# Kernel optimization log

Measured on AMD Instinct MI355X. Metric: run time of the kernel, lower is better.

Reference implementation:

```python
import jax, jax.numpy as jnp
import numpy as np

E = 16        # n_experts
N = 4         # n_mhc
D = 512       # d_hidden
D_FFN = int(D * 1.618)  # 828
TOP_PROB = 0.8
MAX_K = 4
SINKHORN_ITERS = 6
EPS = 1e-8


def top_prob_max_k(logits, threshold=TOP_PROB, max_k=MAX_K):
    probs = jax.nn.softmax(logits, axis=-1)
    order = jnp.argsort(-probs, axis=-1)                       # descending sort indices
    sorted_p = jnp.take_along_axis(probs, order, axis=-1)
    cumsum = jnp.cumsum(sorted_p, axis=-1)
    ar = jnp.arange(logits.shape[-1])
    mask = (cumsum - sorted_p < threshold) & (ar < max_k)
    mask = mask.at[..., 0].set(True)
    selected = sorted_p * mask.astype(probs.dtype)
    inv = jnp.argsort(order, axis=-1)                          # inverse permutation == scatter
    return jnp.take_along_axis(selected, inv, axis=-1)


def sinkhorn_knopp(M, n_iters=SINKHORN_ITERS):
    M = jnp.exp(M)
    for _ in range(n_iters):
        M = M / M.sum(axis=-1, keepdims=True)
        M = M / M.sum(axis=-2, keepdims=True)
    return M


def setup_inputs() -> dict:
    key = jax.random.key(0)
    ks = jax.random.split(key, 12)
    nd = N * D
    inp = {
        'stream': jax.random.normal(ks[0], (2, N, 1024, D), dtype=jnp.float32),
        # BatchedMHC params
        'norm_w': jnp.ones((E, nd), dtype=jnp.float32),
        'phi_pre_w': jax.random.normal(ks[1], (E, N, nd), dtype=jnp.float32) * 0.01,
        'phi_post_w': jax.random.normal(ks[2], (E, N, nd), dtype=jnp.float32) * 0.01,
        'phi_res_w': jax.random.normal(ks[3], (E, N * N, nd), dtype=jnp.float32) * 0.01,
        'b_pre': jnp.zeros((E, N), dtype=jnp.float32),
        'b_post': jnp.zeros((E, N), dtype=jnp.float32),
        'b_res': jnp.zeros((E, N, N), dtype=jnp.float32),
        'alpha_pre': jnp.ones((E,), dtype=jnp.float32),
        'alpha_post': jnp.ones((E,), dtype=jnp.float32),
        'alpha_res': jnp.ones((E,), dtype=jnp.float32),
        # SwiGLU expert params
        'swiglu_norm_w': jnp.ones((E, D), dtype=jnp.float32),
        'swiglu_wd_w': jax.random.normal(ks[4], (E, D, D), dtype=jnp.float32) * 0.01,
        'swiglu_wu_w': jax.random.normal(ks[5], (E, D, D), dtype=jnp.float32) * 0.01,
        'swiglu_gate_w': jax.random.normal(ks[6], (E, D_FFN, D), dtype=jnp.float32) * 0.01,
        'swiglu_up_w': jax.random.normal(ks[7], (E, D_FFN, D), dtype=jnp.float32) * 0.01,
        'swiglu_down_w': jax.random.normal(ks[8], (E, D, D_FFN), dtype=jnp.float32) * 0.01,
        # router (nn.Linear without bias): logits = x @ W.T, W: (E, D)
        'router_w': jax.random.normal(ks[9], (E, D), dtype=jnp.float32) * (1.0 / np.sqrt(D)),
    }
    return inp


def reference(stream, norm_w, phi_pre_w, phi_post_w, phi_res_w,
              b_pre, b_post, b_res, alpha_pre, alpha_post, alpha_res,
              swiglu_norm_w, swiglu_wd_w, swiglu_wu_w,
              swiglu_gate_w, swiglu_up_w, swiglu_down_w, router_w):
    B, n, T, d = stream.shape
    nd = n * d

    # ---- routing (eval mode: no gumbel) ----
    route_input = stream.mean(axis=1)                               # (B,T,d)
    router_logits = jnp.einsum('btd,ed->bte', route_input, router_w)
    gate_moe = top_prob_max_k(router_logits)                        # (B,T,E)
    router_probs = jax.nn.softmax(router_logits, axis=-1)
    moe_mask = (gate_moe > 0).astype(router_probs.dtype)
    route_lp = (jnp.maximum(jnp.log(router_probs), -10.0) * moe_mask).sum(-1)  # (B,T)

    # Original gathers active experts (always excluding expert 0) and skips gate==0
    # experts; since gate_e multiplies each expert's output, computing all experts
    # 1..E-1 is mathematically identical. K = E-1.
    sl = slice(1, E)

    # ---- BatchedMHC ----
    x = stream.transpose(0, 2, 1, 3).reshape(B, T, nd)              # (B,T,nd)
    rms = jax.lax.rsqrt(jnp.mean(x * x, axis=-1, keepdims=True) + EPS)
    xn = x * rms                                                    # (B,T,nd)
    # fold per-expert norm weight into the phi projections (avoids K*B*T*nd tensor)
    phi_pre_eff = phi_pre_w[sl] * norm_w[sl, None, :]               # (K,n,nd)
    phi_post_eff = phi_post_w[sl] * norm_w[sl, None, :]
    phi_res_eff = phi_res_w[sl] * norm_w[sl, None, :]               # (K,n*n,nd)

    H_pre = jax.nn.sigmoid(alpha_pre[sl, None, None, None]
                           * jnp.einsum('btd,knd->kbtn', xn, phi_pre_eff)
                           + b_pre[sl, None, None, :])              # (K,B,T,n)
    H_post = 2.0 * jax.nn.sigmoid(alpha_post[sl, None, None, None]
                                  * jnp.einsum('btd,knd->kbtn', xn, phi_post_eff)
                                  + b_post[sl, None, None, :])      # (K,B,T,n)
    res_e = jnp.einsum('btd,knd->kbtn', xn, phi_res_eff)
    K = E - 1
    H_res_raw = (alpha_res[sl].reshape(K, 1, 1, 1, 1)
                 * res_e.reshape(K, B, T, n, n)
                 + b_res[sl, None, None, :, :])
    H_res = sinkhorn_knopp(H_res_raw)                               # (K,B,T,n,n)

    # ---- per-expert SwiGLU ----
    h_e = jnp.einsum('kbtn,bntd->kbtd', H_pre, stream)              # (K,B,T,d)
    rms2 = jax.lax.rsqrt(jnp.mean(h_e * h_e, axis=-1, keepdims=True) + EPS)
    h = h_e * rms2 * swiglu_norm_w[sl, None, None, :]

    wd_out = jnp.einsum('kbtd,kod->kbto', h, swiglu_wd_w[sl])
    g = jax.nn.sigmoid(jnp.einsum('kbtd,kod->kbto', jax.nn.silu(wd_out), swiglu_wu_w[sl]))
    gate_out = jnp.einsum('kbtd,kod->kbto', h, swiglu_gate_w[sl])   # (K,B,T,d_ffn)
    up_out = jnp.einsum('kbtd,kod->kbto', h, swiglu_up_w[sl])
    out_e = g * jnp.einsum('kbtf,kof->kbto', jax.nn.silu(gate_out) * up_out,
                           swiglu_down_w[sl])                        # (K,B,T,d)

    # ---- combine ----
    gate_4d = gate_moe[:, :, 1:].transpose(2, 0, 1)[:, :, None, :, None]  # (K,B,1,T,1)
    res = jnp.einsum('kbtij,bjtd->kbitd', H_res, stream)            # (K,B,n,T,d)
    post = jnp.einsum('kbtn,kbtd->kbntd', H_post, out_e)            # (K,B,n,T,d)
    stream_update = (gate_4d * (res + post)).sum(axis=0)            # (B,n,T,d)

    return stream_update, gate_moe, route_lp
```

## Files before the change

### kernel.cpp

```cpp
#include <hip/hip_runtime.h>
#include <hip/hip_bf16.h>
#include <math.h>

typedef __attribute__((ext_vector_type(8))) short short8;
typedef __attribute__((ext_vector_type(4))) float floatx4;

#define T_LEN 1024
#define D_H 512
#define ND 2048
#define KEXP 15
#define DFFN 828
#define DFFN_P 896
#define BT_TOT 2048
#define PHI_ROWS 360
#define PHI_ROWS_P 384
#define PAIR_CAP 8320

#define WD_OFF   0
#define WU_OFF   262144
#define GATE_OFF 524288
#define UP_OFF   983040
#define DOWN_OFF 1441792
#define EXPW     1900544

__device__ __forceinline__ float sigmoidf_(float x) { return 1.f / (1.f + expf(-x)); }
__device__ __forceinline__ unsigned short bf16b_(float x) {
    __hip_bfloat16 h = __float2bfloat16(x);
    return *reinterpret_cast<unsigned short*>(&h);
}

__global__ __launch_bounds__(64) void router_kernel(
    const float* __restrict__ stream, const float* __restrict__ rw,
    float* __restrict__ gate_out, float* __restrict__ lp_out,
    int* __restrict__ cnt, int* __restrict__ list, int* __restrict__ pos)
{
    int bt = blockIdx.x; int b = bt >> 10; int t = bt & 1023;
    int lane = threadIdx.x;
    float ri[8];
#pragma unroll
    for (int w = 0; w < 8; ++w) {
        int d = lane + w * 64;
        float s = 0.f;
#pragma unroll
        for (int n = 0; n < 4; ++n)
            s += stream[(((size_t)b * 4 + n) * T_LEN + t) * D_H + d];
        ri[w] = 0.25f * s;
    }
    float logits[16];
    for (int e = 0; e < 16; ++e) {
        float p = 0.f;
#pragma unroll
        for (int w = 0; w < 8; ++w) p += ri[w] * rw[e * D_H + lane + w * 64];
#pragma unroll
        for (int off = 32; off; off >>= 1) p += __shfl_xor(p, off, 64);
        logits[e] = p;
    }
    float mx = logits[0];
    for (int e = 1; e < 16; ++e) mx = fmaxf(mx, logits[e]);
    float pr[16]; float sum = 0.f;
    for (int e = 0; e < 16; ++e) { pr[e] = expf(logits[e] - mx); sum += pr[e]; }
    float inv = 1.f / sum;
    for (int e = 0; e < 16; ++e) pr[e] *= inv;

    float gate[16]; bool taken[16];
    for (int e = 0; e < 16; ++e) { gate[e] = 0.f; taken[e] = false; }
    float prefix = 0.f;
    for (int rank = 0; rank < 4; ++rank) {
        int best = -1; float bp = -1.f;
        for (int e = 0; e < 16; ++e)
            if (!taken[e] && pr[e] > bp) { bp = pr[e]; best = e; }
        taken[best] = true;
        bool sel = (rank == 0) || (prefix < 0.8f);
        if (sel) gate[best] = bp;
        prefix += bp;
        if (!sel) break;
    }
    float lp = 0.f;
    for (int e = 0; e < 16; ++e)
        if (gate[e] > 0.f) lp += fmaxf(logf(pr[e]), -10.f);
    if (lane < 16) gate_out[(size_t)bt * 16 + lane] = gate[lane];
    if (lane == 0) lp_out[bt] = lp;
    if (lane >= 1 && lane < 16 && gate[lane] > 0.f) {
        int k = lane - 1;
        int p = atomicAdd(&cnt[k], 1);
        list[k * BT_TOT + p] = bt;
        pos[k * BT_TOT + bt] = p;
    }
}

__global__ void scan_kernel(const int* __restrict__ cnt, int* __restrict__ offs) {
    if (threadIdx.x == 0) {
        int a = 0;
        for (int k = 0; k < KEXP; ++k) { offs[k] = a; a += cnt[k]; }
        offs[KEXP] = a;
    }
}

__global__ __launch_bounds__(256) void xn_kernel(
    const float* __restrict__ stream, __hip_bfloat16* __restrict__ xn)
{
    int bt = blockIdx.x; int b = bt >> 10; int t = bt & 1023;
    int tid = threadIdx.x;
    float v[8]; float ss = 0.f;
#pragma unroll
    for (int w = 0; w < 8; ++w) {
        int j = tid + w * 256;
        int n = j >> 9, d = j & 511;
        float x = stream[(((size_t)b * 4 + n) * T_LEN + t) * D_H + d];
        v[w] = x; ss += x * x;
    }
#pragma unroll
    for (int off = 32; off; off >>= 1) ss += __shfl_down(ss, off, 64);
    __shared__ float red[4];
    int wave = tid >> 6, lane = tid & 63;
    if (lane == 0) red[wave] = ss;
    __syncthreads();
    float tot = red[0] + red[1] + red[2] + red[3];
    float r = rsqrtf(tot / (float)ND + 1e-8f);
#pragma unroll
    for (int w = 0; w < 8; ++w)
        xn[(size_t)bt * ND + tid + w * 256] = __float2bfloat16(v[w] * r);
}

__global__ __launch_bounds__(256) void cvt_phi_kernel(
    const float* __restrict__ norm_w, const float* __restrict__ phi_pre,
    const float* __restrict__ phi_post, const float* __restrict__ phi_res,
    __hip_bfloat16* __restrict__ phi_all)
{
    int idx = blockIdx.x * 256 + threadIdx.x;
    int row = idx >> 11, col = idx & 2047;
    float v = 0.f;
    if (row < PHI_ROWS) {
        int k = row / 24, j = row - k * 24, e = k + 1;
        float nw = norm_w[(size_t)e * ND + col];
        float p;
        if (j < 4)      p = phi_pre[((size_t)e * 4 + j) * ND + col];
        else if (j < 8) p = phi_post[((size_t)e * 4 + (j - 4)) * ND + col];
        else            p = phi_res[((size_t)e * 16 + (j - 8)) * ND + col];
        v = p * nw;
    }
    phi_all[idx] = __float2bfloat16(v);
}

__global__ __launch_bounds__(256) void cvt_all_kernel(
    const float* __restrict__ wd, const float* __restrict__ wu,
    const float* __restrict__ gate, const float* __restrict__ up,
    const float* __restrict__ down, __hip_bfloat16* __restrict__ wbuf, int e0)
{
    int z = blockIdx.z;
    int type = blockIdx.y;
    int g = blockIdx.x * 256 + threadIdx.x;
    int e = e0 + z;
    __hip_bfloat16* dstb = wbuf + (size_t)z * EXPW;
    float4 v = make_float4(0.f, 0.f, 0.f, 0.f);
    size_t didx;
    if (type <= 1) {
        if (g >= 65536) return;
        didx = (type == 0 ? WD_OFF : WU_OFF) + (size_t)g * 4;
        const float* src = (type == 0 ? wd : wu) + (size_t)e * 262144;
        v = *(const float4*)(src + (size_t)g * 4);
    } else if (type <= 3) {
        if (g >= 114688) return;
        size_t idx4 = (size_t)g * 4;
        didx = (type == 2 ? GATE_OFF : UP_OFF) + idx4;
        if (idx4 < (size_t)DFFN * 512) {
            const float* src = (type == 2 ? gate : up) + (size_t)e * DFFN * 512;
            v = *(const float4*)(src + idx4);
        }
    } else {
        if (g >= 114688) return;
        int r = g / 224, gc = g - r * 224;
        didx = DOWN_OFF + (size_t)g * 4;
        if (gc < 207)
            v = *(const float4*)(down + (size_t)e * 512 * DFFN + (size_t)r * DFFN + gc * 4);
    }
    ushort4 o;
    o.x = bf16b_(v.x); o.y = bf16b_(v.y); o.z = bf16b_(v.z); o.w = bf16b_(v.w);
    *(ushort4*)((unsigned short*)dstb + didx) = o;
}

#define BM 128
#define BN 128
#define BK 32
#define LDSS 40
__global__ __launch_bounds__(256) void gemm_mfma(
    const __hip_bfloat16* __restrict__ A, const __hip_bfloat16* __restrict__ W,
    float* __restrict__ Cf, int Ka, int Oc, int kLen, int kzStride)
{
    __shared__ __align__(16) unsigned short As[BM * LDSS];
    __shared__ __align__(16) unsigned short Ws[BN * LDSS];
    int z = blockIdx.z;
    int bo = blockIdx.x * BN;
    int bm = blockIdx.y * BM;
    int kbeg = z * kzStride;
    int tid = threadIdx.x;
    int wid = tid >> 6, lane = tid & 63;
    int quad = lane >> 4, lr = lane & 15;
    int wm = (wid & 1) * 64, wn = (wid >> 1) * 64;
    int srow = tid >> 2;
    int schk = (tid & 3) * 8;

    floatx4 acc[4][4];
#pragma unroll
    for (int i = 0; i < 4; ++i)
#pragma unroll
        for (int j = 0; j < 4; ++j) { floatx4 zv = {0.f, 0.f, 0.f, 0.f}; acc[i][j] = zv; }

    for (int k0 = kbeg; k0 < kbeg + kLen; k0 += BK) {
        float4 a0 = *(const float4*)(A + (size_t)(bm + srow) * Ka + k0 + schk);
        float4 a1 = *(const float4*)(A + (size_t)(bm + srow + 64) * Ka + k0 + schk);
        float4 w0 = *(const float4*)(W + (size_t)(bo + srow) * Ka + k0 + schk);
        float4 w1 = *(const float4*)(W + (size_t)(bo + srow + 64) * Ka + k0 + schk);
        __syncthreads();
        *(float4*)&As[srow * LDSS + schk] = a0;
        *(float4*)&As[(srow + 64) * LDSS + schk] = a1;
        *(float4*)&Ws[srow * LDSS + schk] = w0;
        *(float4*)&Ws[(srow + 64) * LDSS + schk] = w1;
        __syncthreads();
        short8 af[4], bf[4];
#pragma unroll
        for (int mi = 0; mi < 4; ++mi)
            af[mi] = *(const short8*)&As[(wm + mi * 16 + lr) * LDSS + quad * 8];
#pragma unroll
        for (int ni = 0; ni < 4; ++ni)
            bf[ni] = *(const short8*)&Ws[(wn + ni * 16 + lr) * LDSS + quad * 8];
#pragma unroll
        for (int mi = 0; mi < 4; ++mi)
#pragma unroll
            for (int ni = 0; ni < 4; ++ni)
                acc[mi][ni] = __builtin_amdgcn_mfma_f32_16x16x32_bf16(
                    af[mi], bf[ni], acc[mi][ni], 0, 0, 0);
    }
#pragma unroll
    for (int mi = 0; mi < 4; ++mi) {
        int row0 = bm + wm + mi * 16 + quad * 4;
#pragma unroll
        for (int ni = 0; ni < 4; ++ni) {
            int col = bo + wn + ni * 16 + lr;
#pragma unroll
            for (int r = 0; r < 4; ++r)
                atomicAdd(&Cf[(size_t)(row0 + r) * Oc + col], acc[mi][ni][r]);
        }
    }
}

__global__ __launch_bounds__(256) void gemm_fused(
    const __hip_bfloat16* __restrict__ A, const __hip_bfloat16* __restrict__ wbuf,
    __hip_bfloat16* __restrict__ s1A, __hip_bfloat16* __restrict__ tA,
    const int* __restrict__ counts, const int* __restrict__ offs, int kg)
{
    __shared__ __align__(16) unsigned short As[BM * LDSS];
    __shared__ __align__(16) unsigned short Gs[BN * LDSS];
    __shared__ __align__(16) unsigned short Us[BN * LDSS];
    int z = blockIdx.z;
    int k = kg + z;
    int bm = blockIdx.y * BM;
    if (bm >= counts[k]) return;
    int base = offs[k];
    bool dual = (blockIdx.x >= 4);
    int bo = dual ? (blockIdx.x - 4) * BN : blockIdx.x * BN;
    const __hip_bfloat16* Ab = A + (size_t)base * D_H;
    const __hip_bfloat16* W1 = wbuf + (size_t)z * EXPW + (dual ? GATE_OFF : WD_OFF);
    const __hip_bfloat16* W2 = wbuf + (size_t)z * EXPW + UP_OFF;
    int tid = threadIdx.x;
    int wid = tid >> 6, lane = tid & 63;
    int quad = lane >> 4, lr = lane & 15;
    int wm = (wid & 1) * 64, wn = (wid >> 1) * 64;
    int srow = tid >> 2;
    int schk = (tid & 3) * 8;

    floatx4 a1[4][4], a2[4][4];
#pragma unroll
    for (int i = 0; i < 4; ++i)
#pragma unroll
        for (int j = 0; j < 4; ++j) {
            floatx4 zv = {0.f, 0.f, 0.f, 0.f};
            a1[i][j] = zv; a2[i][j] = zv;
        }

    for (int k0 = 0; k0 < D_H; k0 += BK) {
        float4 x0 = *(const float4*)(Ab + (size_t)(bm + srow) * D_H + k0 + schk);
        float4 x1 = *(const float4*)(Ab + (size_t)(bm + srow + 64) * D_H + k0 + schk);
        float4 g0 = *(const float4*)(W1 + (size_t)(bo + srow) * D_H + k0 + schk);
        float4 g1 = *(const float4*)(W1 + (size_t)(bo + srow + 64) * D_H + k0 + schk);
        float4 u0, u1;
        if (dual) {
            u0 = *(const float4*)(W2 + (size_t)(bo + srow) * D_H + k0 + schk);
            u1 = *(const float4*)(W2 + (size_t)(bo + srow + 64) * D_H + k0 + schk);
        }
        __syncthreads();
        *(float4*)&As[srow * LDSS + schk] = x0;
        *(float4*)&As[(srow + 64) * LDSS + schk] = x1;
        *(float4*)&Gs[srow * LDSS + schk] = g0;
        *(float4*)&Gs[(srow + 64) * LDSS + schk] = g1;
        if (dual) {
            *(float4*)&Us[srow * LDSS + schk] = u0;
            *(float4*)&Us[(srow + 64) * LDSS + schk] = u1;
        }
        __syncthreads();
        short8 af[4], bg[4];
#pragma unroll
        for (int mi = 0; mi < 4; ++mi)
            af[mi] = *(const short8*)&As[(wm + mi * 16 + lr) * LDSS + quad * 8];
#pragma unroll
        for (int ni = 0; ni < 4; ++ni)
            bg[ni] = *(const short8*)&Gs[(wn + ni * 16 + lr) * LDSS + quad * 8];
#pragma unroll
        for (int mi = 0; mi < 4; ++mi)
#pragma unroll
            for (int ni = 0; ni < 4; ++ni)
                a1[mi][ni] = __builtin_amdgcn_mfma_f32_16x16x32_bf16(
                    af[mi], bg[ni], a1[mi][ni], 0, 0, 0);
        if (dual) {
            short8 bu[4];
#pragma unroll
            for (int ni = 0; ni < 4; ++ni)
                bu[ni] = *(const short8*)&Us[(wn + ni * 16 + lr) * LDSS + quad * 8];
#pragma unroll
            for (int mi = 0; mi < 4; ++mi)
#pragma unroll
                for (int ni = 0; ni < 4; ++ni)
                    a2[mi][ni] = __builtin_amdgcn_mfma_f32_16x16x32_bf16(
                        af[mi], bu[ni], a2[mi][ni], 0, 0, 0);
        }
    }

#pragma unroll
    for (int mi = 0; mi < 4; ++mi) {
        int row0 = bm + wm + mi * 16 + quad * 4;
#pragma unroll
        for (int ni = 0; ni < 4; ++ni) {
            int col = bo + wn + ni * 16 + lr;
#pragma unroll
            for (int r = 0; r < 4; ++r) {
                float v = a1[mi][ni][r];
                if (dual) {
                    float uu = a2[mi][ni][r];
                    tA[(size_t)(base + row0 + r) * DFFN_P + col] =
                        __float2bfloat16(v * sigmoidf_(v) * uu);
                } else {
                    s1A[(size_t)(base + row0 + r) * D_H + col] =
                        __float2bfloat16(v * sigmoidf_(v));
                }
            }
        }
    }
}

#define BM64 64
__global__ __launch_bounds__(256) void gemm_mfma64(
    const __hip_bfloat16* __restrict__ A, const __hip_bfloat16* __restrict__ W,
    const __hip_bfloat16* __restrict__ aux, __hip_bfloat16* __restrict__ C,
    const int* __restrict__ counts, const int* __restrict__ offs, int kg,
    int Ka, int Oc, size_t woff, int epi)
{
    __shared__ __align__(16) unsigned short As[BM64 * LDSS];
    __shared__ __align__(16) unsigned short Ws[BN * LDSS];
    int z = blockIdx.z;
    int k = kg + z;
    int bm = blockIdx.y * BM64;
    if (bm >= counts[k]) return;
    int base = offs[k];
    int bo = blockIdx.x * BN;
    const __hip_bfloat16* Ab = A + (size_t)base * Ka;
    const __hip_bfloat16* Wg = W + (size_t)z * EXPW + woff;
    int tid = threadIdx.x;
    int wid = tid >> 6, lane = tid & 63;
    int quad = lane >> 4, lr = lane & 15;
    int wm = (wid & 1) * 32, wn = (wid >> 1) * 64;
    int srow = tid >> 2;
    int schk = (tid & 3) * 8;

    floatx4 acc[2][4];
#pragma unroll
    for (int i = 0; i < 2; ++i)
#pragma unroll
        for (int j = 0; j < 4; ++j) { floatx4 zv = {0.f, 0.f, 0.f, 0.f}; acc[i][j] = zv; }

    for (int k0 = 0; k0 < Ka; k0 += BK) {
        float4 a0 = *(const float4*)(Ab + (size_t)(bm + srow) * Ka + k0 + schk);
        float4 w0 = *(const float4*)(Wg + (size_t)(bo + srow) * Ka + k0 + schk);
        float4 w1 = *(const float4*)(Wg + (size_t)(bo + srow + 64) * Ka + k0 + schk);
        __syncthreads();
        *(float4*)&As[srow * LDSS + schk] = a0;
        *(float4*)&Ws[srow * LDSS + schk] = w0;
        *(float4*)&Ws[(srow + 64) * LDSS + schk] = w1;
        __syncthreads();
        short8 af[2], bf[4];
#pragma unroll
        for (int mi = 0; mi < 2; ++mi)
            af[mi] = *(const short8*)&As[(wm + mi * 16 + lr) * LDSS + quad * 8];
#pragma unroll
        for (int ni = 0; ni < 4; ++ni)
            bf[ni] = *(const short8*)&Ws[(wn + ni * 16 + lr) * LDSS + quad * 8];
#pragma unroll
        for (int mi = 0; mi < 2; ++mi)
#pragma unroll
            for (int ni = 0; ni < 4; ++ni)
                acc[mi][ni] = __builtin_amdgcn_mfma_f32_16x16x32_bf16(
                    af[mi], bf[ni], acc[mi][ni], 0, 0, 0);
    }

#pragma unroll
    for (int mi = 0; mi < 2; ++mi) {
        int row0 = bm + wm + mi * 16 + quad * 4;
#pragma unroll
        for (int ni = 0; ni < 4; ++ni) {
            int col = bo + wn + ni * 16 + lr;
#pragma unroll
            for (int r = 0; r < 4; ++r) {
                float v = acc[mi][ni][r];
                size_t off = (size_t)(base + row0 + r) * Oc + col;
                if (epi == 2) C[off] = __float2bfloat16(sigmoidf_(v));
                else {
                    float a = __bfloat162float(aux[off]);
                    C[off] = __float2bfloat16(a * v);
                }
            }
        }
    }
}

__global__ __launch_bounds__(256) void mhc_post_kernel(
    const float* __restrict__ Cproj,
    const float* __restrict__ b_pre, const float* __restrict__ b_post,
    const float* __restrict__ b_res, const float* __restrict__ a_pre,
    const float* __restrict__ a_post, const float* __restrict__ a_res,
    float* __restrict__ Hpre, float* __restrict__ Hpost, float* __restrict__ Hres)
{
    int gid = blockIdx.x * 256 + threadIdx.x;
    int k = gid >> 11, bt = gid & 2047, e = k + 1;
    const float* s = Cproj + (size_t)bt * PHI_ROWS_P + k * 24;
    float ap = a_pre[e], aq = a_post[e], ar = a_res[e];
#pragma unroll
    for (int n = 0; n < 4; ++n)
        Hpre[((size_t)k * BT_TOT + bt) * 4 + n] = sigmoidf_(ap * s[n] + b_pre[e * 4 + n]);
#pragma unroll
    for (int n = 0; n < 4; ++n)
        Hpost[((size_t)k * BT_TOT + bt) * 4 + n] = 2.f * sigmoidf_(aq * s[4 + n] + b_post[e * 4 + n]);
    float M[16];
#pragma unroll
    for (int i = 0; i < 16; ++i) M[i] = expf(ar * s[8 + i] + b_res[e * 16 + i]);
#pragma unroll
    for (int it = 0; it < 6; ++it) {
#pragma unroll
        for (int i = 0; i < 4; ++i) {
            float iv = 1.f / (M[i*4] + M[i*4+1] + M[i*4+2] + M[i*4+3]);
            M[i*4] *= iv; M[i*4+1] *= iv; M[i*4+2] *= iv; M[i*4+3] *= iv;
        }
#pragma unroll
        for (int j = 0; j < 4; ++j) {
            float iv = 1.f / (M[j] + M[4+j] + M[8+j] + M[12+j]);
            M[j] *= iv; M[4+j] *= iv; M[8+j] *= iv; M[12+j] *= iv;
        }
    }
#pragma unroll
    for (int i = 0; i < 16; ++i) Hres[((size_t)k * BT_TOT + bt) * 16 + i] = M[i];
}

__global__ __launch_bounds__(256) void h_kernel(
    const float* __restrict__ stream, const float* __restrict__ Hpre,
    const float* __restrict__ sw_norm, const int* __restrict__ list,
    const int* __restrict__ counts, const int* __restrict__ offs,
    __hip_bfloat16* __restrict__ hA)
{
    int k = blockIdx.y;
    int i = blockIdx.x;
    if (i >= counts[k]) return;
    int bt = list[k * BT_TOT + i];
    int e = k + 1;
    int b = bt >> 10, t = bt & 1023;
    int tid = threadIdx.x;
    float hp[4];
#pragma unroll
    for (int n = 0; n < 4; ++n) hp[n] = Hpre[((size_t)k * BT_TOT + bt) * 4 + n];
    float he[2]; float ss = 0.f;
#pragma unroll
    for (int w = 0; w < 2; ++w) {
        int d = tid + w * 256;
        float v = 0.f;
#pragma unroll
        for (int n = 0; n < 4; ++n)
            v += hp[n] * stream[(((size_t)b * 4 + n) * T_LEN + t) * D_H + d];
        he[w] = v; ss += v * v;
    }
#pragma unroll
    for (int off = 32; off; off >>= 1) ss += __shfl_down(ss, off, 64);
    __shared__ float red[4];
    int wave = tid >> 6, lane = tid & 63;
    if (lane == 0) red[wave] = ss;
    __syncthreads();
    float tot = red[0] + red[1] + red[2] + red[3];
    float r = rsqrtf(tot / (float)D_H + 1e-8f);
    size_t row = (size_t)(offs[k] + i);
#pragma unroll
    for (int w = 0; w < 2; ++w) {
        int d = tid + w * 256;
        hA[row * D_H + d] = __float2bfloat16(he[w] * r * sw_norm[(size_t)e * D_H + d]);
    }
}

__global__ __launch_bounds__(256) void combine_kernel(
    const float* __restrict__ stream, const __hip_bfloat16* __restrict__ outeA,
    const float* __restrict__ Hpost, const float* __restrict__ Hres,
    const float* __restrict__ gate_all, const int* __restrict__ pos,
    const int* __restrict__ offs, float* __restrict__ out)
{
    int bt = blockIdx.x; int b = bt >> 10; int t = bt & 1023;
    int tid = threadIdx.x;
    float s[2][4], accv[2][4];
#pragma unroll
    for (int w = 0; w < 2; ++w) {
        int d = tid + w * 256;
#pragma unroll
        for (int n = 0; n < 4; ++n) {
            s[w][n] = stream[(((size_t)b * 4 + n) * T_LEN + t) * D_H + d];
            accv[w][n] = 0.f;
        }
    }
    for (int k = 0; k < KEXP; ++k) {
        float gate = gate_all[(size_t)bt * 16 + k + 1];
        if (gate == 0.f) continue;
        size_t row = (size_t)(offs[k] + pos[k * BT_TOT + bt]);
        float hr[16], hp[4];
#pragma unroll
        for (int i = 0; i < 16; ++i) hr[i] = Hres[((size_t)k * BT_TOT + bt) * 16 + i];
#pragma unroll
        for (int i = 0; i < 4; ++i) hp[i] = Hpost[((size_t)k * BT_TOT + bt) * 4 + i];
#pragma unroll
        for (int w = 0; w < 2; ++w) {
            int d = tid + w * 256;
            float oe = __bfloat162float(outeA[row * D_H + d]);
#pragma unroll
            for (int i = 0; i < 4; ++i) {
                float v = hp[i] * oe + hr[i*4+0]*s[w][0] + hr[i*4+1]*s[w][1]
                        + hr[i*4+2]*s[w][2] + hr[i*4+3]*s[w][3];
                accv[w][i] += gate * v;
            }
        }
    }
#pragma unroll
    for (int w = 0; w < 2; ++w) {
        int d = tid + w * 256;
#pragma unroll
        for (int i = 0; i < 4; ++i)
            out[(((size_t)b * 4 + i) * T_LEN + t) * D_H + d] = accv[w][i];
    }
}

extern "C" void kernel_launch(void* const* d_in, const int* in_sizes, int n_in,
                              void* d_out, int out_size, void* d_ws, size_t ws_size,
                              hipStream_t stream) {
    const float* stream_in = (const float*)d_in[0];
    const float* norm_w    = (const float*)d_in[1];
    const float* phi_pre   = (const float*)d_in[2];
    const float* phi_post  = (const float*)d_in[3];
    const float* phi_res   = (const float*)d_in[4];
    const float* b_pre     = (const float*)d_in[5];
    const float* b_post    = (const float*)d_in[6];
    const float* b_res     = (const float*)d_in[7];
    const float* alpha_pre = (const float*)d_in[8];
    const float* alpha_post= (const float*)d_in[9];
    const float* alpha_res = (const float*)d_in[10];
    const float* sw_norm   = (const float*)d_in[11];
    const float* wd_w      = (const float*)d_in[12];
    const float* wu_w      = (const float*)d_in[13];
    const float* gate_w    = (const float*)d_in[14];
    const float* up_w      = (const float*)d_in[15];
    const float* down_w    = (const float*)d_in[16];
    const float* router_w  = (const float*)d_in[17];

    float* out = (float*)d_out;
    const int SU_N = 2 * 4 * T_LEN * D_H;
    float* gate_out = out + SU_N;
    float* lp_out = gate_out + BT_TOT * 16;

    char* p = (char*)d_ws;
    __hip_bfloat16* xn     = (__hip_bfloat16*)p; p += (size_t)BT_TOT * ND * 2;
    __hip_bfloat16* phiall = (__hip_bfloat16*)p; p += (size_t)PHI_ROWS_P * ND * 2;
    float* Cproj = (float*)p; p += (size_t)BT_TOT * PHI_ROWS_P * 4;
    float* Hpre  = (float*)p; p += (size_t)KEXP * BT_TOT * 4 * 4;
    float* Hpost = (float*)p; p += (size_t)KEXP * BT_TOT * 4 * 4;
    float* Hres  = (float*)p; p += (size_t)KEXP * BT_TOT * 16 * 4;
    int* cnt  = (int*)p; p += 256;
    int* offs = (int*)p; p += 256;
    int* list = (int*)p; p += (size_t)KEXP * BT_TOT * 4;
    int* pos  = (int*)p; p += (size_t)KEXP * BT_TOT * 4;
    __hip_bfloat16* hA    = (__hip_bfloat16*)p; p += (size_t)PAIR_CAP * D_H * 2;
    __hip_bfloat16* s1A   = (__hip_bfloat16*)p; p += (size_t)PAIR_CAP * D_H * 2;
    __hip_bfloat16* gA    = (__hip_bfloat16*)p; p += (size_t)PAIR_CAP * D_H * 2;
    __hip_bfloat16* outeA = (__hip_bfloat16*)p; p += (size_t)PAIR_CAP * D_H * 2;
    __hip_bfloat16* tA    = (__hip_bfloat16*)p; p += (size_t)PAIR_CAP * DFFN_P * 2;
    size_t fixed_bytes = (size_t)(p - (char*)d_ws);
    size_t perW = (size_t)EXPW * 2;
    size_t avail = ws_size > fixed_bytes ? ws_size - fixed_bytes : 0;
    int G = (int)(avail / perW);
    if (G > KEXP) G = KEXP;
    if (G < 1) G = 1;
    __hip_bfloat16* wbuf = (__hip_bfloat16*)p;

    hipMemsetAsync(cnt, 0, 64, stream);
    hipMemsetAsync(Cproj, 0, (size_t)BT_TOT * PHI_ROWS_P * 4, stream);
    router_kernel<<<BT_TOT, 64, 0, stream>>>(
        stream_in, router_w, gate_out, lp_out, cnt, list, pos);
    scan_kernel<<<1, 64, 0, stream>>>(cnt, offs);
    xn_kernel<<<BT_TOT, 256, 0, stream>>>(stream_in, xn);
    cvt_phi_kernel<<<(PHI_ROWS_P * ND) / 256, 256, 0, stream>>>(
        norm_w, phi_pre, phi_post, phi_res, phiall);
    gemm_mfma<<<dim3(3, 16, 4), 256, 0, stream>>>(
        xn, phiall, Cproj, ND, PHI_ROWS_P, 512, 512);
    mhc_post_kernel<<<(KEXP * BT_TOT) / 256, 256, 0, stream>>>(
        Cproj, b_pre, b_post, b_res, alpha_pre, alpha_post, alpha_res, Hpre, Hpost, Hres);
    h_kernel<<<dim3(BT_TOT, KEXP), 256, 0, stream>>>(
        stream_in, Hpre, sw_norm, list, cnt, offs, hA);

    for (int kg = 0; kg < KEXP; kg += G) {
        int Gc = (kg + G <= KEXP) ? G : (KEXP - kg);
        int e0 = kg + 1;
        cvt_all_kernel<<<dim3(448, 5, Gc), 256, 0, stream>>>(
            wd_w, wu_w, gate_w, up_w, down_w, wbuf, e0);
        gemm_fused<<<dim3(11, 16, Gc), 256, 0, stream>>>(
            hA, wbuf, s1A, tA, cnt, offs, kg);
        gemm_mfma64<<<dim3(4, 32, Gc), 256, 0, stream>>>(
            s1A, wbuf, nullptr, gA, cnt, offs, kg, 512, 512, WU_OFF, 2);
        gemm_mfma64<<<dim3(4, 32, Gc), 256, 0, stream>>>(
            tA, wbuf, gA, outeA, cnt, offs, kg, DFFN_P, 512, DOWN_OFF, 3);
    }

    combine_kernel<<<BT_TOT, 256, 0, stream>>>(
        stream_in, outeA, Hpost, Hres, gate_out, pos, offs, out);
}
```

Before: 460.4 us.

## Fuse wu and down GEMMs, use direct global-to-LDS loads with swizzle

Merges the two per-expert second-stage GEMMs (wu sigmoid gate and down projection) into one kernel that keeps both accumulators and writes sigmoid(g)*d directly, which removes the gA intermediate buffer and one launch. Stage1 shrinks its M tile to 64 rows and doubles the grid. Both kernels now load tiles with global_load_lds straight into an XOR-swizzled unpadded LDS layout instead of going through registers. Per-expert offsets are padded to multiples of 64 and PAIR_CAP grows to match, so 64-row tiles never cross experts; this costs more registers in the fused kernel and some padded work.

```diff
diff --git a/kernel.cpp b/kernel.cpp
--- a/kernel.cpp
+++ b/kernel.cpp
@@ -14,7 +14,7 @@
 #define BT_TOT 2048
 #define PHI_ROWS 360
 #define PHI_ROWS_P 384
-#define PAIR_CAP 8320
+#define PAIR_CAP 9216
 
 #define WD_OFF   0
 #define WU_OFF   262144
@@ -23,10 +23,19 @@
 #define DOWN_OFF 1441792
 #define EXPW     1900544
 
+#define BK 32
+
 __device__ __forceinline__ float sigmoidf_(float x) { return 1.f / (1.f + expf(-x)); }
 __device__ __forceinline__ unsigned short bf16b_(float x) {
     __hip_bfloat16 h = __float2bfloat16(x);
     return *reinterpret_cast<unsigned short*>(&h);
+}
+
+__device__ __forceinline__ void gload16(const __hip_bfloat16* g, unsigned short* l) {
+    __builtin_amdgcn_global_load_lds(
+        (const __attribute__((address_space(1))) void*)(uintptr_t)g,
+        (__attribute__((address_space(3))) void*)(unsigned int)(uintptr_t)l,
+        16, 0, 0);
 }
 
 __global__ __launch_bounds__(64) void router_kernel(
@@ -91,7 +100,7 @@
 __global__ void scan_kernel(const int* __restrict__ cnt, int* __restrict__ offs) {
     if (threadIdx.x == 0) {
         int a = 0;
-        for (int k = 0; k < KEXP; ++k) { offs[k] = a; a += cnt[k]; }
+        for (int k = 0; k < KEXP; ++k) { offs[k] = a; a += (cnt[k] + 63) & ~63; }
         offs[KEXP] = a;
     }
 }
@@ -179,19 +188,16 @@
     *(ushort4*)((unsigned short*)dstb + didx) = o;
 }
 
-#define BM 128
-#define BN 128
-#define BK 32
 #define LDSS 40
-__global__ __launch_bounds__(256) void gemm_mfma(
+__global__ __launch_bounds__(256) void gemm_dense(
     const __hip_bfloat16* __restrict__ A, const __hip_bfloat16* __restrict__ W,
     float* __restrict__ Cf, int Ka, int Oc, int kLen, int kzStride)
 {
-    __shared__ __align__(16) unsigned short As[BM * LDSS];
-    __shared__ __align__(16) unsigned short Ws[BN * LDSS];
+    __shared__ __align__(16) unsigned short As[128 * LDSS];
+    __shared__ __align__(16) unsigned short Ws[128 * LDSS];
     int z = blockIdx.z;
-    int bo = blockIdx.x * BN;
-    int bm = blockIdx.y * BM;
+    int bo = blockIdx.x * 128;
+    int bm = blockIdx.y * 128;
     int kbeg = z * kzStride;
     int tid = threadIdx.x;
     int wid = tid >> 6, lane = tid & 63;
@@ -244,69 +250,66 @@
     }
 }
 
-__global__ __launch_bounds__(256) void gemm_fused(
-    const __hip_bfloat16* __restrict__ A, const __hip_bfloat16* __restrict__ wbuf,
+__global__ __launch_bounds__(256) void gemm_stage1(
+    const __hip_bfloat16* __restrict__ hA, const __hip_bfloat16* __restrict__ wbuf,
     __hip_bfloat16* __restrict__ s1A, __hip_bfloat16* __restrict__ tA,
-    const int* __restrict__ counts, const int* __restrict__ offs, int kg)
-{
-    __shared__ __align__(16) unsigned short As[BM * LDSS];
-    __shared__ __align__(16) unsigned short Gs[BN * LDSS];
-    __shared__ __align__(16) unsigned short Us[BN * LDSS];
+    const int* __restrict__ cnt, const int* __restrict__ offs, int kg)
+{
+    __shared__ __align__(16) unsigned short As[64 * 32];
+    __shared__ __align__(16) unsigned short Gs[128 * 32];
+    __shared__ __align__(16) unsigned short Us[128 * 32];
     int z = blockIdx.z;
     int k = kg + z;
-    int bm = blockIdx.y * BM;
-    if (bm >= counts[k]) return;
+    int bm = blockIdx.y * 64;
+    if (bm >= cnt[k]) return;
     int base = offs[k];
     bool dual = (blockIdx.x >= 4);
-    int bo = dual ? (blockIdx.x - 4) * BN : blockIdx.x * BN;
-    const __hip_bfloat16* Ab = A + (size_t)base * D_H;
+    int bo = (dual ? (blockIdx.x - 4) : blockIdx.x) * 128;
+    const __hip_bfloat16* Ab = hA + (size_t)base * D_H;
     const __hip_bfloat16* W1 = wbuf + (size_t)z * EXPW + (dual ? GATE_OFF : WD_OFF);
     const __hip_bfloat16* W2 = wbuf + (size_t)z * EXPW + UP_OFF;
     int tid = threadIdx.x;
     int wid = tid >> 6, lane = tid & 63;
     int quad = lane >> 4, lr = lane & 15;
-    int wm = (wid & 1) * 64, wn = (wid >> 1) * 64;
-    int srow = tid >> 2;
-    int schk = (tid & 3) * 8;
-
-    floatx4 a1[4][4], a2[4][4];
-#pragma unroll
-    for (int i = 0; i < 4; ++i)
+    int lrow = lane >> 2, lchk = lane & 3;
+    int achk = lchk ^ ((lrow >> 1) & 3);
+    int fs = quad ^ ((lr >> 1) & 3);
+    int wm = (wid & 1) * 32, wn = (wid >> 1) * 64;
+
+    floatx4 a1[2][4], a2[2][4];
+#pragma unroll
+    for (int i = 0; i < 2; ++i)
 #pragma unroll
         for (int j = 0; j < 4; ++j) {
             floatx4 zv = {0.f, 0.f, 0.f, 0.f};
             a1[i][j] = zv; a2[i][j] = zv;
         }
 
+    int sr0 = wid * 16 + lrow;
+    int sr1 = (wid + 4) * 16 + lrow;
+    const size_t aoff  = (size_t)(bm + sr0) * D_H + achk * 8;
+    const size_t g0off = (size_t)(bo + sr0) * D_H + achk * 8;
+    const size_t g1off = (size_t)(bo + sr1) * D_H + achk * 8;
+
     for (int k0 = 0; k0 < D_H; k0 += BK) {
-        float4 x0 = *(const float4*)(Ab + (size_t)(bm + srow) * D_H + k0 + schk);
-        float4 x1 = *(const float4*)(Ab + (size_t)(bm + srow + 64) * D_H + k0 + schk);
-        float4 g0 = *(const float4*)(W1 + (size_t)(bo + srow) * D_H + k0 + schk);
-        float4 g1 = *(const float4*)(W1 + (size_t)(bo + srow + 64) * D_H + k0 + schk);
-        float4 u0, u1;
+        __syncthreads();
+        gload16(Ab + aoff + k0, As + wid * 512);
+        gload16(W1 + g0off + k0, Gs + wid * 512);
+        gload16(W1 + g1off + k0, Gs + (wid + 4) * 512);
         if (dual) {
-            u0 = *(const float4*)(W2 + (size_t)(bo + srow) * D_H + k0 + schk);
-            u1 = *(const float4*)(W2 + (size_t)(bo + srow + 64) * D_H + k0 + schk);
-        }
-        __syncthreads();
-        *(float4*)&As[srow * LDSS + schk] = x0;
-        *(float4*)&As[(srow + 64) * LDSS + schk] = x1;
-        *(float4*)&Gs[srow * LDSS + schk] = g0;
-        *(float4*)&Gs[(srow + 64) * LDSS + schk] = g1;
-        if (dual) {
-            *(float4*)&Us[srow * LDSS + schk] = u0;
-            *(float4*)&Us[(srow + 64) * LDSS + schk] = u1;
-        }
-        __syncthreads();
-        short8 af[4], bg[4];
-#pragma unroll
-        for (int mi = 0; mi < 4; ++mi)
-            af[mi] = *(const short8*)&As[(wm + mi * 16 + lr) * LDSS + quad * 8];
+            gload16(W2 + g0off + k0, Us + wid * 512);
+            gload16(W2 + g1off + k0, Us + (wid + 4) * 512);
+        }
+        __syncthreads();
+        short8 af[2], bg[4];
+#pragma unroll
+        for (int mi = 0; mi < 2; ++mi)
+            af[mi] = *(const short8*)&As[(wm + mi * 16 + lr) * 32 + fs * 8];
 #pragma unroll
         for (int ni = 0; ni < 4; ++ni)
-            bg[ni] = *(const short8*)&Gs[(wn + ni * 16 + lr) * LDSS + quad * 8];
-#pragma unroll
-        for (int mi = 0; mi < 4; ++mi)
+            bg[ni] = *(const short8*)&Gs[(wn + ni * 16 + lr) * 32 + fs * 8];
+#pragma unroll
+        for (int mi = 0; mi < 2; ++mi)
 #pragma unroll
             for (int ni = 0; ni < 4; ++ni)
                 a1[mi][ni] = __builtin_amdgcn_mfma_f32_16x16x32_bf16(
@@ -315,9 +318,9 @@
             short8 bu[4];
 #pragma unroll
             for (int ni = 0; ni < 4; ++ni)
-                bu[ni] = *(const short8*)&Us[(wn + ni * 16 + lr) * LDSS + quad * 8];
-#pragma unroll
-            for (int mi = 0; mi < 4; ++mi)
+                bu[ni] = *(const short8*)&Us[(wn + ni * 16 + lr) * 32 + fs * 8];
+#pragma unroll
+            for (int mi = 0; mi < 2; ++mi)
 #pragma unroll
                 for (int ni = 0; ni < 4; ++ni)
                     a2[mi][ni] = __builtin_amdgcn_mfma_f32_16x16x32_bf16(
@@ -326,7 +329,7 @@
     }
 
 #pragma unroll
-    for (int mi = 0; mi < 4; ++mi) {
+    for (int mi = 0; mi < 2; ++mi) {
         int row0 = bm + wm + mi * 16 + quad * 4;
 #pragma unroll
         for (int ni = 0; ni < 4; ++ni) {
@@ -347,58 +350,81 @@
     }
 }
 
-#define BM64 64
-__global__ __launch_bounds__(256) void gemm_mfma64(
-    const __hip_bfloat16* __restrict__ A, const __hip_bfloat16* __restrict__ W,
-    const __hip_bfloat16* __restrict__ aux, __hip_bfloat16* __restrict__ C,
-    const int* __restrict__ counts, const int* __restrict__ offs, int kg,
-    int Ka, int Oc, size_t woff, int epi)
-{
-    __shared__ __align__(16) unsigned short As[BM64 * LDSS];
-    __shared__ __align__(16) unsigned short Ws[BN * LDSS];
+__global__ __launch_bounds__(256) void gemm_final(
+    const __hip_bfloat16* __restrict__ s1A, const __hip_bfloat16* __restrict__ tA,
+    const __hip_bfloat16* __restrict__ wbuf, __hip_bfloat16* __restrict__ outeA,
+    const int* __restrict__ cnt, const int* __restrict__ offs, int kg)
+{
+    __shared__ __align__(16) unsigned short As[64 * 32];
+    __shared__ __align__(16) unsigned short Ws[128 * 32];
     int z = blockIdx.z;
     int k = kg + z;
-    int bm = blockIdx.y * BM64;
-    if (bm >= counts[k]) return;
+    int bm = blockIdx.y * 64;
+    if (bm >= cnt[k]) return;
     int base = offs[k];
-    int bo = blockIdx.x * BN;
-    const __hip_bfloat16* Ab = A + (size_t)base * Ka;
-    const __hip_bfloat16* Wg = W + (size_t)z * EXPW + woff;
+    int bo = blockIdx.x * 128;
+    const __hip_bfloat16* A1 = s1A + (size_t)base * D_H;
+    const __hip_bfloat16* A2 = tA + (size_t)base * DFFN_P;
+    const __hip_bfloat16* Wu = wbuf + (size_t)z * EXPW + WU_OFF;
+    const __hip_bfloat16* Wd = wbuf + (size_t)z * EXPW + DOWN_OFF;
     int tid = threadIdx.x;
     int wid = tid >> 6, lane = tid & 63;
     int quad = lane >> 4, lr = lane & 15;
+    int lrow = lane >> 2, lchk = lane & 3;
+    int achk = lchk ^ ((lrow >> 1) & 3);
+    int fs = quad ^ ((lr >> 1) & 3);
     int wm = (wid & 1) * 32, wn = (wid >> 1) * 64;
-    int srow = tid >> 2;
-    int schk = (tid & 3) * 8;
-
-    floatx4 acc[2][4];
+    int sr0 = wid * 16 + lrow;
+    int sr1 = (wid + 4) * 16 + lrow;
+
+    floatx4 accg[2][4], accd[2][4];
 #pragma unroll
     for (int i = 0; i < 2; ++i)
 #pragma unroll
-        for (int j = 0; j < 4; ++j) { floatx4 zv = {0.f, 0.f, 0.f, 0.f}; acc[i][j] = zv; }
-
-    for (int k0 = 0; k0 < Ka; k0 += BK) {
-        float4 a0 = *(const float4*)(Ab + (size_t)(bm + srow) * Ka + k0 + schk);
-        float4 w0 = *(const float4*)(Wg + (size_t)(bo + srow) * Ka + k0 + schk);
-        float4 w1 = *(const float4*)(Wg + (size_t)(bo + srow + 64) * Ka + k0 + schk);
-        __syncthreads();
-        *(float4*)&As[srow * LDSS + schk] = a0;
-        *(float4*)&Ws[srow * LDSS + schk] = w0;
-        *(float4*)&Ws[(srow + 64) * LDSS + schk] = w1;
+        for (int j = 0; j < 4; ++j) {
+            floatx4 zv = {0.f, 0.f, 0.f, 0.f};
+            accg[i][j] = zv; accd[i][j] = zv;
+        }
+
+    for (int k0 = 0; k0 < D_H; k0 += BK) {
+        __syncthreads();
+        gload16(A1 + (size_t)(bm + sr0) * D_H + k0 + achk * 8, As + wid * 512);
+        gload16(Wu + (size_t)(bo + sr0) * D_H + k0 + achk * 8, Ws + wid * 512);
+        gload16(Wu + (size_t)(bo + sr1) * D_H + k0 + achk * 8, Ws + (wid + 4) * 512);
         __syncthreads();
         short8 af[2], bf[4];
 #pragma unroll
         for (int mi = 0; mi < 2; ++mi)
-            af[mi] = *(const short8*)&As[(wm + mi * 16 + lr) * LDSS + quad * 8];
+            af[mi] = *(const short8*)&As[(wm + mi * 16 + lr) * 32 + fs * 8];
 #pragma unroll
         for (int ni = 0; ni < 4; ++ni)
-            bf[ni] = *(const short8*)&Ws[(wn + ni * 16 + lr) * LDSS + quad * 8];
+            bf[ni] = *(const short8*)&Ws[(wn + ni * 16 + lr) * 32 + fs * 8];
 #pragma unroll
         for (int mi = 0; mi < 2; ++mi)
 #pragma unroll
             for (int ni = 0; ni < 4; ++ni)
-                acc[mi][ni] = __builtin_amdgcn_mfma_f32_16x16x32_bf16(
-                    af[mi], bf[ni], acc[mi][ni], 0, 0, 0);
+                accg[mi][ni] = __builtin_amdgcn_mfma_f32_16x16x32_bf16(
+                    af[mi], bf[ni], accg[mi][ni], 0, 0, 0);
+    }
+    for (int k0 = 0; k0 < DFFN_P; k0 += BK) {
+        __syncthreads();
+        gload16(A2 + (size_t)(bm + sr0) * DFFN_P + k0 + achk * 8, As + wid * 512);
+        gload16(Wd + (size_t)(bo + sr0) * DFFN_P + k0 + achk * 8, Ws + wid * 512);
+        gload16(Wd + (size_t)(bo + sr1) * DFFN_P + k0 + achk * 8, Ws + (wid + 4) * 512);
+        __syncthreads();
+        short8 af[2], bf[4];
+#pragma unroll
+        for (int mi = 0; mi < 2; ++mi)
+            af[mi] = *(const short8*)&As[(wm + mi * 16 + lr) * 32 + fs * 8];
+#pragma unroll
+        for (int ni = 0; ni < 4; ++ni)
+            bf[ni] = *(const short8*)&Ws[(wn + ni * 16 + lr) * 32 + fs * 8];
+#pragma unroll
+        for (int mi = 0; mi < 2; ++mi)
+#pragma unroll
+            for (int ni = 0; ni < 4; ++ni)
+                accd[mi][ni] = __builtin_amdgcn_mfma_f32_16x16x32_bf16(
+                    af[mi], bf[ni], accd[mi][ni], 0, 0, 0);
     }
 
 #pragma unroll
@@ -409,13 +435,10 @@
             int col = bo + wn + ni * 16 + lr;
 #pragma unroll
             for (int r = 0; r < 4; ++r) {
-                float v = acc[mi][ni][r];
-                size_t off = (size_t)(base + row0 + r) * Oc + col;
-                if (epi == 2) C[off] = __float2bfloat16(sigmoidf_(v));
-                else {
-                    float a = __bfloat162float(aux[off]);
-                    C[off] = __float2bfloat16(a * v);
-                }
+                float g = accg[mi][ni][r];
+                float d = accd[mi][ni][r];
+                outeA[(size_t)(base + row0 + r) * D_H + col] =
+                    __float2bfloat16(sigmoidf_(g) * d);
             }
         }
     }
@@ -588,7 +611,6 @@
     int* pos  = (int*)p; p += (size_t)KEXP * BT_TOT * 4;
     __hip_bfloat16* hA    = (__hip_bfloat16*)p; p += (size_t)PAIR_CAP * D_H * 2;
     __hip_bfloat16* s1A   = (__hip_bfloat16*)p; p += (size_t)PAIR_CAP * D_H * 2;
-    __hip_bfloat16* gA    = (__hip_bfloat16*)p; p += (size_t)PAIR_CAP * D_H * 2;
     __hip_bfloat16* outeA = (__hip_bfloat16*)p; p += (size_t)PAIR_CAP * D_H * 2;
     __hip_bfloat16* tA    = (__hip_bfloat16*)p; p += (size_t)PAIR_CAP * DFFN_P * 2;
     size_t fixed_bytes = (size_t)(p - (char*)d_ws);
@@ -607,7 +629,7 @@
     xn_kernel<<<BT_TOT, 256, 0, stream>>>(stream_in, xn);
     cvt_phi_kernel<<<(PHI_ROWS_P * ND) / 256, 256, 0, stream>>>(
         norm_w, phi_pre, phi_post, phi_res, phiall);
-    gemm_mfma<<<dim3(3, 16, 4), 256, 0, stream>>>(
+    gemm_dense<<<dim3(3, 16, 4), 256, 0, stream>>>(
         xn, phiall, Cproj, ND, PHI_ROWS_P, 512, 512);
     mhc_post_kernel<<<(KEXP * BT_TOT) / 256, 256, 0, stream>>>(
         Cproj, b_pre, b_post, b_res, alpha_pre, alpha_post, alpha_res, Hpre, Hpost, Hres);
@@ -619,12 +641,10 @@
         int e0 = kg + 1;
         cvt_all_kernel<<<dim3(448, 5, Gc), 256, 0, stream>>>(
             wd_w, wu_w, gate_w, up_w, down_w, wbuf, e0);
-        gemm_fused<<<dim3(11, 16, Gc), 256, 0, stream>>>(
+        gemm_stage1<<<dim3(11, 32, Gc), 256, 0, stream>>>(
             hA, wbuf, s1A, tA, cnt, offs, kg);
-        gemm_mfma64<<<dim3(4, 32, Gc), 256, 0, stream>>>(
-            s1A, wbuf, nullptr, gA, cnt, offs, kg, 512, 512, WU_OFF, 2);
-        gemm_mfma64<<<dim3(4, 32, Gc), 256, 0, stream>>>(
-            tA, wbuf, gA, outeA, cnt, offs, kg, DFFN_P, 512, DOWN_OFF, 3);
+        gemm_final<<<dim3(4, 32, Gc), 256, 0, stream>>>(
+            s1A, tA, wbuf, outeA, cnt, offs, kg);
     }
 
     combine_kernel<<<BT_TOT, 256, 0, stream>>>(
```

Result: faster. 400.3 us (-13.1%).
